# Performance work log

Hardware: AMD Instinct MI355X
Metric: run time of the kernel (lower is better)

Reference implementation:

```python
import jax, jax.numpy as jnp
import numpy as np

MODEL_DIM = 1024
NUM_HEADS = 16
D_K = MODEL_DIM // NUM_HEADS  # 64
MAX_SEQ_LEN = 4096


def _xavier(key, shape):
    fan_in, fan_out = shape[1], shape[0]
    limit = np.sqrt(6.0 / (fan_in + fan_out)).astype(np.float32)
    return jax.random.uniform(key, shape, jnp.float32, -limit, limit)


def setup_inputs() -> dict:
    key = jax.random.key(0)
    ks = jax.random.split(key, 6)
    x = jax.random.normal(ks[0], (2, 2048, MODEL_DIM), jnp.float32)
    wq = _xavier(ks[1], (MODEL_DIM, MODEL_DIM))
    wk = _xavier(ks[2], (MODEL_DIM, MODEL_DIM))
    wv = _xavier(ks[3], (MODEL_DIM, MODEL_DIM))
    wo = _xavier(ks[4], (MODEL_DIM, MODEL_DIM))
    bq = jnp.zeros((MODEL_DIM,), jnp.float32)
    bk = jnp.zeros((MODEL_DIM,), jnp.float32)
    bv = jnp.zeros((MODEL_DIM,), jnp.float32)
    bo = jnp.zeros((MODEL_DIM,), jnp.float32)
    # precomputed rotary tables (cos/sin of position * theta^(-2i/d))
    half = D_K // 2
    theta = jnp.power(10000.0, jnp.arange(half, dtype=jnp.float32) * (-2.0 / D_K))
    angles = jnp.arange(MAX_SEQ_LEN, dtype=jnp.float32)[:, None] * theta[None, :]
    rot_cos = jnp.cos(angles)  # [max_seq_len, d_k//2]
    rot_sin = jnp.sin(angles)
    return {"x": x, "wq": wq, "bq": bq, "wk": wk, "bk": bk,
            "wv": wv, "bv": bv, "wo": wo, "bo": bo,
            "rot_cos": rot_cos, "rot_sin": rot_sin}


def reference(x, wq, bq, wk, bk, wv, bv, wo, bo, rot_cos, rot_sin):
    b, t, m = x.shape
    h, d = NUM_HEADS, m // NUM_HEADS
    # NOTE: original uses .view (reshape), NOT transpose, to split heads.
    q = (x @ wq.T + bq).reshape(b, h, t, d)
    k = (x @ wk.T + bk).reshape(b, h, t, d)
    v = (x @ wv.T + bv).reshape(b, h, t, d)
    # Faithful to original: rotation matrix indexed by scalar position == seq_len,
    # so every token uses the SAME rotation angle (position t).
    c = rot_cos[t]  # [d//2]
    s = rot_sin[t]

    def rope(u):
        ur = u.reshape(b, h, t, d // 2, 2)
        re, im = ur[..., 0], ur[..., 1]
        return jnp.stack([re * c - im * s, re * s + im * c], axis=-1).reshape(b, h, t, d)

    q, k = rope(q), rope(k)
    scores = jnp.einsum('bhqd,bhkd->bhqk', q, k) / np.float32(np.sqrt(d))
    p = jax.nn.softmax(scores, axis=-1)  # mask='none', dropout=0.0
    o = jnp.einsum('bhqk,bhkd->bhqd', p, v)
    o = o.transpose(0, 2, 1, 3).reshape(b, t, m)  # 'b h t d -> b t (h d)'
    return o @ wo.T + bo
```

## Files before the change

### kernel.cpp

```cpp
#include <hip/hip_runtime.h>
#include <hip/hip_bf16.h>
#include <stdint.h>


typedef __attribute__((ext_vector_type(8))) short bf16x8;
typedef bf16x8 __attribute__((may_alias)) bf16x8_a;
typedef __attribute__((ext_vector_type(4))) float f32x4;
typedef __attribute__((ext_vector_type(2))) unsigned int u32x2;
typedef u32x2 __attribute__((may_alias)) u32x2_a;

__device__ inline unsigned short f2b(float f) {
  union { float f; unsigned int u; } x; x.f = f;
  unsigned int r = x.u + 0x7fffu + ((x.u >> 16) & 1u);
  return (unsigned short)(r >> 16);
}

__device__ inline unsigned cvtpk_bf16(float lo, float hi) {
  unsigned r;
  asm("v_cvt_pk_bf16_f32 %0, %1, %2" : "=v"(r) : "v"(lo), "v"(hi));
  return r;
}

__global__ __launch_bounds__(256) void cvt_all(
    const float* __restrict__ x,
    const float* __restrict__ w0, const float* __restrict__ w1,
    const float* __restrict__ w2, const float* __restrict__ w3,
    unsigned short* __restrict__ xb,
    unsigned short* __restrict__ o0, unsigned short* __restrict__ o1,
    unsigned short* __restrict__ o2, unsigned short* __restrict__ o3) {
  int bid = blockIdx.x;
  const float* in; unsigned short* out; int i;
  if (bid < 4096) { in = x; out = xb; i = bid * 256 + threadIdx.x; }
  else {
    int w = (bid - 4096) >> 10;
    in = (w == 0) ? w0 : (w == 1) ? w1 : (w == 2) ? w2 : w3;
    out = (w == 0) ? o0 : (w == 1) ? o1 : (w == 2) ? o2 : o3;
    i = ((bid - 4096) & 1023) * 256 + threadIdx.x;
  }
  float4 v = reinterpret_cast<const float4*>(in)[i];
  ushort4 o;
  o.x = f2b(v.x); o.y = f2b(v.y); o.z = f2b(v.z); o.w = f2b(v.w);
  reinterpret_cast<ushort4*>(out)[i] = o;
}

template<int MODE>
__global__ __launch_bounds__(256) void gemm_bt(
    const unsigned short* __restrict__ A,
    const unsigned short* __restrict__ W0, const unsigned short* __restrict__ W1,
    const float* __restrict__ b0, const float* __restrict__ b1,
    unsigned short* __restrict__ o0, unsigned short* __restrict__ o1,
    float* __restrict__ of, int M, int N, int K)
{
  const int tid = threadIdx.x;
  const int lane = tid & 63;
  const int wid = tid >> 6;
  const int q4 = lane >> 4;
  const int l15 = lane & 15;
  const int wr = wid >> 1, wc = wid & 1;

  const unsigned short* W = W0; const float* bias = b0; unsigned short* ob = o0;
  if (MODE == 0 && blockIdx.z == 1) { W = W1; bias = b1; ob = o1; }

  __shared__ __align__(16) unsigned short sA[2][128 * 64];
  __shared__ __align__(16) unsigned short sB[2][128 * 64];
  char* sAc = (char*)sA;
  char* sBc = (char*)sB;

  f32x4 acc[4][4];
#pragma unroll
  for (int i = 0; i < 4; ++i)
#pragma unroll
    for (int j = 0; j < 4; ++j) acc[i][j] = (f32x4){0.f, 0.f, 0.f, 0.f};

  const size_t rowA0 = (size_t)blockIdx.x * 128;
  const size_t rowB0 = (size_t)blockIdx.y * 128;

  auto stage = [&](int bs, int k0) {
#pragma unroll
    for (int it = 0; it < 4; ++it) {
      int Loff = it * 4096 + wid * 1024;
      int L = Loff + lane * 16;
      int row = L >> 7;
      int csrc = ((L >> 4) & 7) ^ (row & 7);
      const unsigned short* ga = A + (rowA0 + row) * K + k0 + csrc * 8;
      const unsigned short* gw = W + (rowB0 + row) * K + k0 + csrc * 8;
      __builtin_amdgcn_global_load_lds((const __attribute__((address_space(1))) void*)ga,
                                       (__attribute__((address_space(3))) void*)(sAc + bs * 16384 + Loff),
                                       16, 0, 0);
      __builtin_amdgcn_global_load_lds((const __attribute__((address_space(1))) void*)gw,
                                       (__attribute__((address_space(3))) void*)(sBc + bs * 16384 + Loff),
                                       16, 0, 0);
    }
  };

  stage(0, 0);

  const int NT = K >> 6;
  for (int t = 0; t < NT; ++t) {
    const int cur = t & 1;
    __syncthreads();
    if (t + 1 < NT) stage(cur ^ 1, (t + 1) * 64);

#pragma unroll
    for (int ks = 0; ks < 2; ++ks) {
      bf16x8 af[4], bfr[4];
#pragma unroll
      for (int f = 0; f < 4; ++f) {
        int ra = wr * 64 + f * 16 + l15;
        af[f] = *(const bf16x8_a*)(sAc + cur * 16384 + ra * 128 +
                                   ((ks * 64 + q4 * 16) ^ ((ra & 7) << 4)));
        int rb = wc * 64 + f * 16 + l15;
        bfr[f] = *(const bf16x8_a*)(sBc + cur * 16384 + rb * 128 +
                                    ((ks * 64 + q4 * 16) ^ ((rb & 7) << 4)));
      }
      __builtin_amdgcn_s_setprio(1);
#pragma unroll
      for (int i = 0; i < 4; ++i)
#pragma unroll
        for (int j = 0; j < 4; ++j) {
          if (MODE == 2)
            acc[i][j] = __builtin_amdgcn_mfma_f32_16x16x32_bf16(bfr[j], af[i], acc[i][j], 0, 0, 0);
          else
            acc[i][j] = __builtin_amdgcn_mfma_f32_16x16x32_bf16(af[i], bfr[j], acc[i][j], 0, 0, 0);
        }
      __builtin_amdgcn_s_setprio(0);
    }
  }

  if (MODE == 2) {
    const int bh = (int)rowA0 >> 7;
#pragma unroll
    for (int i = 0; i < 4; ++i) {
      const int tt = wr * 64 + i * 16 + l15;
      const size_t rb = (size_t)bh * 131072 + tt;
#pragma unroll
      for (int j = 0; j < 4; ++j) {
#pragma unroll
        for (int r = 0; r < 4; ++r) {
          const int c = (int)rowB0 + wc * 64 + j * 16 + q4 * 4 + r;
          ob[rb + (size_t)(c & 63) * 2048 + (size_t)(c >> 6) * 128] = f2b(acc[i][j][r] + bias[c]);
        }
      }
    }
  } else {
#pragma unroll
    for (int i = 0; i < 4; ++i) {
      int row = (int)rowA0 + wr * 64 + i * 16 + q4 * 4;
#pragma unroll
      for (int j = 0; j < 4; ++j) {
        int col = (int)rowB0 + wc * 64 + j * 16 + l15;
        float bv = bias[col];
        if (MODE == 0 && blockIdx.z == 1) {
#pragma unroll
          for (int r = 0; r < 4; ++r) {
            size_t a = (size_t)((row + r) >> 7) * 131072 +
                       (size_t)(((col >> 6) << 7) + ((row + r) & 127)) * 64 + (col & 63);
            ob[a] = f2b(acc[i][j][r] + bv);
          }
        } else {
#pragma unroll
          for (int r = 0; r < 4; ++r) {
            float v = acc[i][j][r] + bv;
            if (MODE == 0) ob[(size_t)(row + r) * N + col] = f2b(v * 0.18033688f);
            else           of[(size_t)(row + r) * N + col] = v;
          }
        }
      }
    }
  }
}

__global__ __launch_bounds__(256, 2) void attn_kernel(
    const unsigned short* __restrict__ Qg,
    const unsigned short* __restrict__ Kg,
    const unsigned short* __restrict__ VTg,
    unsigned short* __restrict__ ctx)
{
  const int tid = threadIdx.x;
  const int lane = tid & 63;
  const int wid = tid >> 6;
  const int q4 = lane >> 4;
  const int l15 = lane & 15;

  const int bid = blockIdx.x;
  const int bh = (bid & 7) * 4 + ((bid >> 3) >> 4);
  const int qt = (bid >> 3) & 15;
  const int b = bh >> 4, h = bh & 15;
  const size_t base = (size_t)bh * 131072;
  const unsigned short* Qh = Qg + base;
  const unsigned short* Kh = Kg + base;
  const unsigned short* VTh = VTg + base;
  const int q0 = qt * 128;

  __shared__ __align__(16) unsigned short sK[2][128 * 64];
  __shared__ __align__(16) unsigned short sV[2][128 * 64];
  __shared__ __align__(16) unsigned short sP[4][32 * 64];

  bf16x8 qf[2][2];
#pragma unroll
  for (int s = 0; s < 2; ++s)
#pragma unroll
    for (int ks = 0; ks < 2; ++ks)
      qf[s][ks] = *(const bf16x8*)(Qh + (size_t)(q0 + wid * 32 + s * 16 + l15) * 64 + ks * 32 + q4 * 8);

  const int rr = tid >> 3;
  const int colB = ((tid & 7) ^ (rr & 7)) * 8;
  const unsigned short* gK = Kh + (size_t)rr * 64 + colB;
  const unsigned short* gV = VTh + (size_t)rr * 2048 + colB;
  char* sKc = (char*)sK;
  char* sVc = (char*)sV;
  char* sPw = (char*)sP + wid * 4096;

  auto stage = [&](int bs, int kv0) {
#pragma unroll
    for (int hf = 0; hf < 2; ++hf) {
      const int kvh = kv0 + hf * 64;
      char* dK = sKc + bs * 16384 + hf * 8192 + wid * 1024;
      char* dV = sVc + bs * 16384 + hf * 8192 + wid * 1024;
      __builtin_amdgcn_global_load_lds(
          (const __attribute__((address_space(1))) void*)(gK + (size_t)kvh * 64),
          (__attribute__((address_space(3))) void*)dK, 16, 0, 0);
      __builtin_amdgcn_global_load_lds(
          (const __attribute__((address_space(1))) void*)(gK + (size_t)kvh * 64 + 2048),
          (__attribute__((address_space(3))) void*)(dK + 4096), 16, 0, 0);
      __builtin_amdgcn_global_load_lds(
          (const __attribute__((address_space(1))) void*)(gV + kvh),
          (__attribute__((address_space(3))) void*)dV, 16, 0, 0);
      __builtin_amdgcn_global_load_lds(
          (const __attribute__((address_space(1))) void*)(gV + kvh + 65536),
          (__attribute__((address_space(3))) void*)(dV + 4096), 16, 0, 0);
    }
  };

  f32x4 oacc[2][4];
#pragma unroll
  for (int s = 0; s < 2; ++s)
#pragma unroll
    for (int fn = 0; fn < 4; ++fn) oacc[s][fn] = (f32x4){0.f, 0.f, 0.f, 0.f};
  float m_run[2] = {-INFINITY, -INFINITY};
  float l_run[2] = {0.f, 0.f};

  stage(0, 0);

  for (int t = 0; t < 16; ++t) {
    const int cur = t & 1;
    __syncthreads();
    if (t < 15) stage(cur ^ 1, (t + 1) * 128);

#pragma unroll
    for (int hf = 0; hf < 2; ++hf) {
      const int bbase = cur * 16384 + hf * 8192;

      f32x4 sc[2][4];
#pragma unroll
      for (int s = 0; s < 2; ++s)
#pragma unroll
        for (int fm = 0; fm < 4; ++fm) sc[s][fm] = (f32x4){0.f, 0.f, 0.f, 0.f};
      __builtin_amdgcn_s_setprio(1);
#pragma unroll
      for (int ks = 0; ks < 2; ++ks) {
#pragma unroll
        for (int fm = 0; fm < 4; ++fm) {
          const int rk = fm * 16 + l15;
          bf16x8_a kf = *(const bf16x8_a*)(sKc + bbase + rk * 128 +
                                           ((ks * 64 + q4 * 16) ^ ((rk & 7) << 4)));
          sc[0][fm] = __builtin_amdgcn_mfma_f32_16x16x32_bf16(kf, qf[0][ks], sc[0][fm], 0, 0, 0);
          sc[1][fm] = __builtin_amdgcn_mfma_f32_16x16x32_bf16(kf, qf[1][ks], sc[1][fm], 0, 0, 0);
        }
      }
      __builtin_amdgcn_s_setprio(0);

#pragma unroll
      for (int s = 0; s < 2; ++s) {
        float mx = fmaxf(fmaxf(fmaxf(sc[s][0][0], sc[s][0][1]), fmaxf(sc[s][0][2], sc[s][0][3])),
                         fmaxf(fmaxf(sc[s][1][0], sc[s][1][1]), fmaxf(sc[s][1][2], sc[s][1][3])));
        mx = fmaxf(mx, fmaxf(fmaxf(fmaxf(sc[s][2][0], sc[s][2][1]), fmaxf(sc[s][2][2], sc[s][2][3])),
                             fmaxf(fmaxf(sc[s][3][0], sc[s][3][1]), fmaxf(sc[s][3][2], sc[s][3][3]))));
        mx = fmaxf(mx, __shfl_xor(mx, 16));
        mx = fmaxf(mx, __shfl_xor(mx, 32));
        if (!__all(mx <= m_run[s] + 11.54f)) {
          const float mnew = fmaxf(m_run[s], mx);
          const float sc_o = __builtin_amdgcn_exp2f(m_run[s] - mnew);
          l_run[s] *= sc_o;
          m_run[s] = mnew;
#pragma unroll
          for (int r = 0; r < 4; ++r) {
            const float so = __shfl(sc_o, (lane & 48) | (q4 * 4 + r));
#pragma unroll
            for (int fn = 0; fn < 4; ++fn) oacc[s][fn][r] *= so;
          }
        }
        float rs = 0.f;
#pragma unroll
        for (int fm = 0; fm < 4; ++fm)
#pragma unroll
          for (int r = 0; r < 4; ++r) {
            sc[s][fm][r] = __builtin_amdgcn_exp2f(sc[s][fm][r] - m_run[s]);
            rs += sc[s][fm][r];
          }
        rs += __shfl_xor(rs, 16);
        rs += __shfl_xor(rs, 32);
        l_run[s] += rs;

        char* rowp = sPw + (s * 16 + l15) * 128;
#pragma unroll
        for (int fm = 0; fm < 4; ++fm) {
          u32x2 pk;
          pk[0] = cvtpk_bf16(sc[s][fm][0], sc[s][fm][1]);
          pk[1] = cvtpk_bf16(sc[s][fm][2], sc[s][fm][3]);
          *(u32x2_a*)(rowp + ((fm * 32 + q4 * 8) ^ ((l15 & 7) << 4))) = pk;
        }
      }
      asm volatile("s_waitcnt lgkmcnt(0)" ::: "memory");
      __builtin_amdgcn_sched_barrier(0);

#pragma unroll
      for (int ks2 = 0; ks2 < 2; ++ks2) {
        bf16x8 pf[2];
#pragma unroll
        for (int s = 0; s < 2; ++s)
          pf[s] = *(const bf16x8_a*)(sPw + (s * 16 + l15) * 128 +
                                     ((ks2 * 64 + q4 * 16) ^ ((l15 & 7) << 4)));
        __builtin_amdgcn_s_setprio(1);
#pragma unroll
        for (int fn = 0; fn < 4; ++fn) {
          const int rv = fn * 16 + l15;
          bf16x8_a vf = *(const bf16x8_a*)(sVc + bbase + rv * 128 +
                                           ((ks2 * 64 + q4 * 16) ^ ((rv & 7) << 4)));
          oacc[0][fn] = __builtin_amdgcn_mfma_f32_16x16x32_bf16(pf[0], vf, oacc[0][fn], 0, 0, 0);
          oacc[1][fn] = __builtin_amdgcn_mfma_f32_16x16x32_bf16(pf[1], vf, oacc[1][fn], 0, 0, 0);
        }
        __builtin_amdgcn_s_setprio(0);
      }
    }
  }

#pragma unroll
  for (int s = 0; s < 2; ++s) {
    const float inv = 1.0f / l_run[s];
#pragma unroll
    for (int r = 0; r < 4; ++r) {
      const float ir = __shfl(inv, (lane & 48) | (q4 * 4 + r));
      const int trow = q0 + wid * 32 + s * 16 + q4 * 4 + r;
      const size_t ro = ((size_t)b * 2048 + trow) * 1024 + h * 64;
#pragma unroll
      for (int fn = 0; fn < 4; ++fn)
        ctx[ro + fn * 16 + l15] = f2b(oacc[s][fn][r] * ir);
    }
  }
}

extern "C" void kernel_launch(void* const* d_in, const int* in_sizes, int n_in,
                              void* d_out, int out_size, void* d_ws, size_t ws_size,
                              hipStream_t stream) {
  const float* x  = (const float*)d_in[0];
  const float* wq = (const float*)d_in[1];
  const float* bq = (const float*)d_in[2];
  const float* wk = (const float*)d_in[3];
  const float* bk = (const float*)d_in[4];
  const float* wv = (const float*)d_in[5];
  const float* bv = (const float*)d_in[6];
  const float* wo = (const float*)d_in[7];
  const float* bo = (const float*)d_in[8];

  char* ws = (char*)d_ws;
  unsigned short* xb  = (unsigned short*)(ws);
  unsigned short* wqb = (unsigned short*)(ws + 8388608);
  unsigned short* wkb = (unsigned short*)(ws + 10485760);
  unsigned short* wvb = (unsigned short*)(ws + 12582912);
  unsigned short* wob = (unsigned short*)(ws + 14680064);
  unsigned short* Qb  = (unsigned short*)(ws + 16777216);
  unsigned short* Kb  = (unsigned short*)(ws + 25165824);
  unsigned short* VTb = (unsigned short*)(ws + 33554432);
  unsigned short* ctx = xb;

  cvt_all<<<8192, 256, 0, stream>>>(x, wq, wk, wv, wo, xb, wqb, wkb, wvb, wob);

  gemm_bt<0><<<dim3(32, 8, 2), 256, 0, stream>>>(
      xb, wqb, wkb, bq, bk, Qb, Kb, nullptr, 4096, 1024, 1024);
  gemm_bt<2><<<dim3(32, 8, 1), 256, 0, stream>>>(
      xb, wvb, nullptr, bv, nullptr, VTb, nullptr, nullptr, 4096, 1024, 1024);

  attn_kernel<<<dim3(512), dim3(256), 0, stream>>>(Qb, Kb, VTb, ctx);

  gemm_bt<1><<<dim3(32, 8, 1), 256, 0, stream>>>(
      ctx, wob, nullptr, bo, nullptr, nullptr, nullptr,
      (float*)d_out, 4096, 1024, 1024);
}
```

Measured before the change: 132.6 us.

## Split attention KV range across two wave groups with in-block softmax merge

```diff
diff --git a/kernel.cpp b/kernel.cpp
--- a/kernel.cpp
+++ b/kernel.cpp
@@ -6,6 +6,7 @@
 typedef __attribute__((ext_vector_type(8))) short bf16x8;
 typedef bf16x8 __attribute__((may_alias)) bf16x8_a;
 typedef __attribute__((ext_vector_type(4))) float f32x4;
+typedef f32x4 __attribute__((may_alias)) f32x4_a;
 typedef __attribute__((ext_vector_type(2))) unsigned int u32x2;
 typedef u32x2 __attribute__((may_alias)) u32x2_a;
 
@@ -170,7 +171,7 @@
   }
 }
 
-__global__ __launch_bounds__(256, 2) void attn_kernel(
+__global__ __launch_bounds__(512, 4) void attn_kernel(
     const unsigned short* __restrict__ Qg,
     const unsigned short* __restrict__ Kg,
     const unsigned short* __restrict__ VTg,
@@ -179,6 +180,8 @@
   const int tid = threadIdx.x;
   const int lane = tid & 63;
   const int wid = tid >> 6;
+  const int half = wid >> 2;
+  const int wq = wid & 3;
   const int q4 = lane >> 4;
   const int l15 = lane & 15;
 
@@ -191,45 +194,37 @@
   const unsigned short* Kh = Kg + base;
   const unsigned short* VTh = VTg + base;
   const int q0 = qt * 128;
-
-  __shared__ __align__(16) unsigned short sK[2][128 * 64];
-  __shared__ __align__(16) unsigned short sV[2][128 * 64];
-  __shared__ __align__(16) unsigned short sP[4][32 * 64];
+  const int kvbase = half * 1024;
+
+  __shared__ __align__(16) char smem[49152];
+  char* sKc = smem;
+  char* sVc = smem + 16384;
+  char* sPw = smem + 32768 + wid * 2048;
 
   bf16x8 qf[2][2];
 #pragma unroll
   for (int s = 0; s < 2; ++s)
 #pragma unroll
     for (int ks = 0; ks < 2; ++ks)
-      qf[s][ks] = *(const bf16x8*)(Qh + (size_t)(q0 + wid * 32 + s * 16 + l15) * 64 + ks * 32 + q4 * 8);
-
-  const int rr = tid >> 3;
-  const int colB = ((tid & 7) ^ (rr & 7)) * 8;
-  const unsigned short* gK = Kh + (size_t)rr * 64 + colB;
-  const unsigned short* gV = VTh + (size_t)rr * 2048 + colB;
-  char* sKc = (char*)sK;
-  char* sVc = (char*)sV;
-  char* sPw = (char*)sP + wid * 4096;
-
-  auto stage = [&](int bs, int kv0) {
-#pragma unroll
-    for (int hf = 0; hf < 2; ++hf) {
-      const int kvh = kv0 + hf * 64;
-      char* dK = sKc + bs * 16384 + hf * 8192 + wid * 1024;
-      char* dV = sVc + bs * 16384 + hf * 8192 + wid * 1024;
-      __builtin_amdgcn_global_load_lds(
-          (const __attribute__((address_space(1))) void*)(gK + (size_t)kvh * 64),
-          (__attribute__((address_space(3))) void*)dK, 16, 0, 0);
-      __builtin_amdgcn_global_load_lds(
-          (const __attribute__((address_space(1))) void*)(gK + (size_t)kvh * 64 + 2048),
-          (__attribute__((address_space(3))) void*)(dK + 4096), 16, 0, 0);
-      __builtin_amdgcn_global_load_lds(
-          (const __attribute__((address_space(1))) void*)(gV + kvh),
-          (__attribute__((address_space(3))) void*)dV, 16, 0, 0);
-      __builtin_amdgcn_global_load_lds(
-          (const __attribute__((address_space(1))) void*)(gV + kvh + 65536),
-          (__attribute__((address_space(3))) void*)(dV + 4096), 16, 0, 0);
-    }
+      qf[s][ks] = *(const bf16x8*)(Qh + (size_t)(q0 + wq * 32 + s * 16 + l15) * 64 + ks * 32 + q4 * 8);
+
+  const int u = tid & 255;
+  const int rK = u >> 3;
+  const int cK = ((u & 7) ^ (rK & 7)) * 8;
+  const unsigned short* gK = Kh + (size_t)(kvbase + rK) * 64 + cK;
+  const int rV = u >> 2;
+  const int cV = ((u & 3) ^ (rV & 3)) * 8;
+  const unsigned short* gV = VTh + (size_t)rV * 2048 + kvbase + cV;
+
+  auto stage = [&](int bs, int t) {
+    char* dK = sKc + half * 8192 + bs * 4096 + wq * 1024;
+    char* dV = sVc + half * 8192 + bs * 4096 + wq * 1024;
+    __builtin_amdgcn_global_load_lds(
+        (const __attribute__((address_space(1))) void*)(gK + (size_t)t * 2048),
+        (__attribute__((address_space(3))) void*)dK, 16, 0, 0);
+    __builtin_amdgcn_global_load_lds(
+        (const __attribute__((address_space(1))) void*)(gV + t * 32),
+        (__attribute__((address_space(3))) void*)dV, 16, 0, 0);
   };
 
   f32x4 oacc[2][4];
@@ -242,110 +237,133 @@
 
   stage(0, 0);
 
-  for (int t = 0; t < 16; ++t) {
+  for (int t = 0; t < 32; ++t) {
     const int cur = t & 1;
     __syncthreads();
-    if (t < 15) stage(cur ^ 1, (t + 1) * 128);
-
-#pragma unroll
-    for (int hf = 0; hf < 2; ++hf) {
-      const int bbase = cur * 16384 + hf * 8192;
-
-      f32x4 sc[2][4];
+    if (t < 31) stage(cur ^ 1, t + 1);
+
+    char* kbuf = sKc + half * 8192 + cur * 4096;
+    char* vbuf = sVc + half * 8192 + cur * 4096;
+
+    f32x4 sc[2][2];
+#pragma unroll
+    for (int s = 0; s < 2; ++s)
+#pragma unroll
+      for (int fm = 0; fm < 2; ++fm) sc[s][fm] = (f32x4){0.f, 0.f, 0.f, 0.f};
+    __builtin_amdgcn_s_setprio(1);
+#pragma unroll
+    for (int ks = 0; ks < 2; ++ks) {
+#pragma unroll
+      for (int fm = 0; fm < 2; ++fm) {
+        const int rk = fm * 16 + l15;
+        bf16x8_a kf = *(const bf16x8_a*)(kbuf + rk * 128 +
+                                         ((ks * 64 + q4 * 16) ^ ((rk & 7) << 4)));
+        sc[0][fm] = __builtin_amdgcn_mfma_f32_16x16x32_bf16(kf, qf[0][ks], sc[0][fm], 0, 0, 0);
+        sc[1][fm] = __builtin_amdgcn_mfma_f32_16x16x32_bf16(kf, qf[1][ks], sc[1][fm], 0, 0, 0);
+      }
+    }
+    __builtin_amdgcn_s_setprio(0);
+
+#pragma unroll
+    for (int s = 0; s < 2; ++s) {
+      float mx = fmaxf(fmaxf(fmaxf(sc[s][0][0], sc[s][0][1]), fmaxf(sc[s][0][2], sc[s][0][3])),
+                       fmaxf(fmaxf(sc[s][1][0], sc[s][1][1]), fmaxf(sc[s][1][2], sc[s][1][3])));
+      mx = fmaxf(mx, __shfl_xor(mx, 16));
+      mx = fmaxf(mx, __shfl_xor(mx, 32));
+      if (!__all(mx <= m_run[s] + 11.54f)) {
+        const float mnew = fmaxf(m_run[s], mx);
+        const float sc_o = __builtin_amdgcn_exp2f(m_run[s] - mnew);
+        l_run[s] *= sc_o;
+        m_run[s] = mnew;
+#pragma unroll
+        for (int r = 0; r < 4; ++r) {
+          const float so = __shfl(sc_o, (lane & 48) | (q4 * 4 + r));
+#pragma unroll
+          for (int fn = 0; fn < 4; ++fn) oacc[s][fn][r] *= so;
+        }
+      }
+      float rs = 0.f;
+#pragma unroll
+      for (int fm = 0; fm < 2; ++fm)
+#pragma unroll
+        for (int r = 0; r < 4; ++r) {
+          sc[s][fm][r] = __builtin_amdgcn_exp2f(sc[s][fm][r] - m_run[s]);
+          rs += sc[s][fm][r];
+        }
+      rs += __shfl_xor(rs, 16);
+      rs += __shfl_xor(rs, 32);
+      l_run[s] += rs;
+
+      const int prow = s * 16 + l15;
+      char* rowp = sPw + prow * 64;
+#pragma unroll
+      for (int fm = 0; fm < 2; ++fm) {
+        u32x2 pk;
+        pk[0] = cvtpk_bf16(sc[s][fm][0], sc[s][fm][1]);
+        pk[1] = cvtpk_bf16(sc[s][fm][2], sc[s][fm][3]);
+        const int c = fm * 2 + (q4 >> 1);
+        *(u32x2_a*)(rowp + ((c ^ (prow & 3)) << 4) + (q4 & 1) * 8) = pk;
+      }
+    }
+    asm volatile("s_waitcnt lgkmcnt(0)" ::: "memory");
+    __builtin_amdgcn_sched_barrier(0);
+
+    bf16x8 pf[2];
+#pragma unroll
+    for (int s = 0; s < 2; ++s) {
+      const int prow = s * 16 + l15;
+      pf[s] = *(const bf16x8_a*)(sPw + prow * 64 + ((q4 ^ (prow & 3)) << 4));
+    }
+    __builtin_amdgcn_s_setprio(1);
+#pragma unroll
+    for (int fn = 0; fn < 4; ++fn) {
+      const int rv = fn * 16 + l15;
+      bf16x8_a vf = *(const bf16x8_a*)(vbuf + rv * 64 + ((q4 ^ (rv & 3)) << 4));
+      oacc[0][fn] = __builtin_amdgcn_mfma_f32_16x16x32_bf16(pf[0], vf, oacc[0][fn], 0, 0, 0);
+      oacc[1][fn] = __builtin_amdgcn_mfma_f32_16x16x32_bf16(pf[1], vf, oacc[1][fn], 0, 0, 0);
+    }
+    __builtin_amdgcn_s_setprio(0);
+  }
+
+  __syncthreads();
+  if (half == 1) {
+    char* mb = smem + wq * 8192;
+#pragma unroll
+    for (int s = 0; s < 2; ++s)
+#pragma unroll
+      for (int fn = 0; fn < 4; ++fn)
+        *(f32x4_a*)(mb + (((s * 4 + fn) * 64) + lane) * 16) = oacc[s][fn];
+    if (q4 == 0) {
 #pragma unroll
       for (int s = 0; s < 2; ++s)
-#pragma unroll
-        for (int fm = 0; fm < 4; ++fm) sc[s][fm] = (f32x4){0.f, 0.f, 0.f, 0.f};
-      __builtin_amdgcn_s_setprio(1);
-#pragma unroll
-      for (int ks = 0; ks < 2; ++ks) {
-#pragma unroll
-        for (int fm = 0; fm < 4; ++fm) {
-          const int rk = fm * 16 + l15;
-          bf16x8_a kf = *(const bf16x8_a*)(sKc + bbase + rk * 128 +
-                                           ((ks * 64 + q4 * 16) ^ ((rk & 7) << 4)));
-          sc[0][fm] = __builtin_amdgcn_mfma_f32_16x16x32_bf16(kf, qf[0][ks], sc[0][fm], 0, 0, 0);
-          sc[1][fm] = __builtin_amdgcn_mfma_f32_16x16x32_bf16(kf, qf[1][ks], sc[1][fm], 0, 0, 0);
-        }
-      }
-      __builtin_amdgcn_s_setprio(0);
-
-#pragma unroll
-      for (int s = 0; s < 2; ++s) {
-        float mx = fmaxf(fmaxf(fmaxf(sc[s][0][0], sc[s][0][1]), fmaxf(sc[s][0][2], sc[s][0][3])),
-                         fmaxf(fmaxf(sc[s][1][0], sc[s][1][1]), fmaxf(sc[s][1][2], sc[s][1][3])));
-        mx = fmaxf(mx, fmaxf(fmaxf(fmaxf(sc[s][2][0], sc[s][2][1]), fmaxf(sc[s][2][2], sc[s][2][3])),
-                             fmaxf(fmaxf(sc[s][3][0], sc[s][3][1]), fmaxf(sc[s][3][2], sc[s][3][3]))));
-        mx = fmaxf(mx, __shfl_xor(mx, 16));
-        mx = fmaxf(mx, __shfl_xor(mx, 32));
-        if (!__all(mx <= m_run[s] + 11.54f)) {
-          const float mnew = fmaxf(m_run[s], mx);
-          const float sc_o = __builtin_amdgcn_exp2f(m_run[s] - mnew);
-          l_run[s] *= sc_o;
-          m_run[s] = mnew;
-#pragma unroll
-          for (int r = 0; r < 4; ++r) {
-            const float so = __shfl(sc_o, (lane & 48) | (q4 * 4 + r));
-#pragma unroll
-            for (int fn = 0; fn < 4; ++fn) oacc[s][fn][r] *= so;
-          }
-        }
-        float rs = 0.f;
-#pragma unroll
-        for (int fm = 0; fm < 4; ++fm)
-#pragma unroll
-          for (int r = 0; r < 4; ++r) {
-            sc[s][fm][r] = __builtin_amdgcn_exp2f(sc[s][fm][r] - m_run[s]);
-            rs += sc[s][fm][r];
-          }
-        rs += __shfl_xor(rs, 16);
-        rs += __shfl_xor(rs, 32);
-        l_run[s] += rs;
-
-        char* rowp = sPw + (s * 16 + l15) * 128;
-#pragma unroll
-        for (int fm = 0; fm < 4; ++fm) {
-          u32x2 pk;
-          pk[0] = cvtpk_bf16(sc[s][fm][0], sc[s][fm][1]);
-          pk[1] = cvtpk_bf16(sc[s][fm][2], sc[s][fm][3]);
-          *(u32x2_a*)(rowp + ((fm * 32 + q4 * 8) ^ ((l15 & 7) << 4))) = pk;
-        }
-      }
-      asm volatile("s_waitcnt lgkmcnt(0)" ::: "memory");
-      __builtin_amdgcn_sched_barrier(0);
-
-#pragma unroll
-      for (int ks2 = 0; ks2 < 2; ++ks2) {
-        bf16x8 pf[2];
-#pragma unroll
-        for (int s = 0; s < 2; ++s)
-          pf[s] = *(const bf16x8_a*)(sPw + (s * 16 + l15) * 128 +
-                                     ((ks2 * 64 + q4 * 16) ^ ((l15 & 7) << 4)));
-        __builtin_amdgcn_s_setprio(1);
+        *(float2*)(smem + 32768 + ((wq * 2 + s) * 16 + l15) * 8) =
+            make_float2(m_run[s], l_run[s]);
+    }
+  }
+  __syncthreads();
+  if (half == 0) {
+    char* mb = smem + wq * 8192;
+#pragma unroll
+    for (int s = 0; s < 2; ++s) {
+      float2 ml = *(const float2*)(smem + 32768 + ((wq * 2 + s) * 16 + l15) * 8);
+      const float mm = fmaxf(m_run[s], ml.x);
+      const float w1 = __builtin_amdgcn_exp2f(m_run[s] - mm);
+      const float w2 = __builtin_amdgcn_exp2f(ml.x - mm);
+      const float li = 1.0f / (l_run[s] * w1 + ml.y * w2);
+#pragma unroll
+      for (int r = 0; r < 4; ++r) {
+        const int src = (lane & 48) | (q4 * 4 + r);
+        const float w1b = __shfl(w1, src);
+        const float w2b = __shfl(w2, src);
+        const float lib = __shfl(li, src);
+        const int trow = q0 + wq * 32 + s * 16 + q4 * 4 + r;
+        const size_t ro = ((size_t)b * 2048 + trow) * 1024 + h * 64;
 #pragma unroll
         for (int fn = 0; fn < 4; ++fn) {
-          const int rv = fn * 16 + l15;
-          bf16x8_a vf = *(const bf16x8_a*)(sVc + bbase + rv * 128 +
-                                           ((ks2 * 64 + q4 * 16) ^ ((rv & 7) << 4)));
-          oacc[0][fn] = __builtin_amdgcn_mfma_f32_16x16x32_bf16(pf[0], vf, oacc[0][fn], 0, 0, 0);
-          oacc[1][fn] = __builtin_amdgcn_mfma_f32_16x16x32_bf16(pf[1], vf, oacc[1][fn], 0, 0, 0);
-        }
-        __builtin_amdgcn_s_setprio(0);
-      }
-    }
-  }
-
-#pragma unroll
-  for (int s = 0; s < 2; ++s) {
-    const float inv = 1.0f / l_run[s];
-#pragma unroll
-    for (int r = 0; r < 4; ++r) {
-      const float ir = __shfl(inv, (lane & 48) | (q4 * 4 + r));
-      const int trow = q0 + wid * 32 + s * 16 + q4 * 4 + r;
-      const size_t ro = ((size_t)b * 2048 + trow) * 1024 + h * 64;
-#pragma unroll
-      for (int fn = 0; fn < 4; ++fn)
-        ctx[ro + fn * 16 + l15] = f2b(oacc[s][fn][r] * ir);
+          f32x4 o2 = *(const f32x4_a*)(mb + (((s * 4 + fn) * 64) + lane) * 16);
+          ctx[ro + fn * 16 + l15] = f2b((oacc[s][fn][r] * w1b + o2[r] * w2b) * lib);
+        }
+      }
     }
   }
 }
@@ -381,7 +399,7 @@
   gemm_bt<2><<<dim3(32, 8, 1), 256, 0, stream>>>(
       xb, wvb, nullptr, bv, nullptr, VTb, nullptr, nullptr, 4096, 1024, 1024);
 
-  attn_kernel<<<dim3(512), dim3(256), 0, stream>>>(Qb, Kb, VTb, ctx);
+  attn_kernel<<<dim3(512), dim3(512), 0, stream>>>(Qb, Kb, VTb, ctx);
 
   gemm_bt<1><<<dim3(32, 8, 1), 256, 0, stream>>>(
       ctx, wob, nullptr, bo, nullptr, nullptr, nullptr,
```

New measurement: 133.8 us. Within noise of the previous version (+0.8%).
